# Performance work log

Hardware: AMD Instinct MI355X
Metric: run time of the kernel (lower is better)

## Reference

```python
import jax, jax.numpy as jnp
import numpy as np

INPUT_LEN = 256
LATENT = 128
B, T = 64, 1024
# layer (in_dim, units): encoder: (256,256),(256,128); decoder: (128,256),(256,256)
LAYERS = [(INPUT_LEN, 2 * LATENT), (2 * LATENT, LATENT), (LATENT, 2 * LATENT), (2 * LATENT, INPUT_LEN)]


def _lstm_relu(xs, W, U, b):
    """Keras LSTM with activation='relu', recurrent_activation='sigmoid'.
    xs: [B,T,F]; W: [F,4H]; U: [H,4H]; b: [4H]; gate order i,f,g,o. Returns [B,T,H]."""
    Bsz = xs.shape[0]
    H = U.shape[0]
    h0 = jnp.zeros((Bsz, H), xs.dtype)
    c0 = jnp.zeros((Bsz, H), xs.dtype)
    # precompute input projection for all timesteps: [T,B,4H]
    zx = jnp.einsum('btf,fg->tbg', xs, W) + b

    def step(carry, zx_t):
        h, c = carry
        z = zx_t + h @ U
        i, f, g, o = jnp.split(z, 4, axis=-1)
        i = jax.nn.sigmoid(i)
        f = jax.nn.sigmoid(f)
        o = jax.nn.sigmoid(o)
        g = jax.nn.relu(g)
        c = f * c + i * g
        h = o * jax.nn.relu(c)
        return (h, c), h

    _, hs = jax.lax.scan(step, (h0, c0), zx)  # hs: [T,B,H]
    return jnp.swapaxes(hs, 0, 1)


def setup_inputs() -> dict:
    key = jax.random.key(0)
    ks = jax.random.split(key, 1 + 3 * len(LAYERS))
    d = {"x": jax.random.normal(ks[0], (B, T, INPUT_LEN), dtype=jnp.float32)}
    for li, (fin, h) in enumerate(LAYERS):
        kW, kU, kb = ks[1 + 3 * li], ks[2 + 3 * li], ks[3 + 3 * li]
        d[f"W{li+1}"] = jax.random.normal(kW, (fin, 4 * h), dtype=jnp.float32) * 0.05
        d[f"U{li+1}"] = jax.random.normal(kU, (h, 4 * h), dtype=jnp.float32) * 0.05
        d[f"b{li+1}"] = jnp.zeros((4 * h,), dtype=jnp.float32)
    return d


def reference(x, W1, U1, b1, W2, U2, b2, W3, U3, b3, W4, U4, b4):
    h = _lstm_relu(x, W1, U1, b1)   # encoder layer 1: [B,T,256]
    h = _lstm_relu(h, W2, U2, b2)   # encoder layer 2: [B,T,128]
    h = _lstm_relu(h, W3, U3, b3)   # decoder layer 1: [B,T,256]
    h = _lstm_relu(h, W4, U4, b4)   # decoder layer 2: [B,T,256]
    return h
```

## Files before the change

### kernel.cpp

```cpp
#include <hip/hip_runtime.h>
#include <hip/hip_bf16.h>


typedef __bf16 bf16x8 __attribute__((ext_vector_type(8)));
typedef float f32x4 __attribute__((ext_vector_type(4)));

#define NWG 56
#define TSTEPS 1024
#define NSTEPS (TSTEPS + 3)

__device__ __forceinline__ f32x4 mfma16(bf16x8 a, bf16x8 b, f32x4 c) {
  return __builtin_amdgcn_mfma_f32_16x16x32_bf16(a, b, c, 0, 0, 0);
}

__device__ __forceinline__ float sigmoid_fast(float x) {
  return 1.0f / (1.0f + __expf(-x));
}

__device__ __forceinline__ void grid_barrier(unsigned* flags, int wg,
                                             unsigned target) {
  __syncthreads();
  if (threadIdx.x < 64) {
    __threadfence();
    if (threadIdx.x == 0)
      __hip_atomic_store(&flags[wg * 32], target, __ATOMIC_RELAXED,
                         __HIP_MEMORY_SCOPE_AGENT);
    const int idx = (threadIdx.x < NWG) ? (int)threadIdx.x : 0;
    while (true) {
      unsigned v = __hip_atomic_load(&flags[idx * 32], __ATOMIC_RELAXED,
                                     __HIP_MEMORY_SCOPE_AGENT);
      if (!__ballot(v < target)) break;
      __builtin_amdgcn_s_sleep(1);
    }
    __threadfence();
  }
  __syncthreads();
}

template <int F, int H, int LAYER>
__device__ void layer_loop(const float* __restrict__ xg,
                           const __bf16* __restrict__ xin,
                           const float* __restrict__ W,
                           const float* __restrict__ U,
                           const float* __restrict__ bias_g,
                           __bf16* __restrict__ hbuf,
                           float* __restrict__ out,
                           unsigned* flags, int wg, int slice, __bf16* smem) {
  constexpr int KW = F / 32;
  constexpr int KU = H / 32;
  constexpr int FOURH = 4 * H;
  const int tid = threadIdx.x;
  const int wave = tid >> 6;
  const int lane = tid & 63;
  const int l15 = lane & 15;
  const int q = lane >> 4;
  const int hcol = slice * 16 + l15;
  const int brow = wave * 16;

  float bz[4];
#pragma unroll
  for (int nt = 0; nt < 4; ++nt) bz[nt] = bias_g[nt * H + hcol];

  bf16x8 wf[4][KW];
  bf16x8 uf[4][KU];
  for (int idx = tid; idx < F * 64; idx += 256) {
    int k = idx >> 6, c = idx & 63;
    int col = (c >> 4) * H + slice * 16 + (c & 15);
    smem[c * F + k] = (__bf16)W[k * FOURH + col];
  }
  __syncthreads();
#pragma unroll
  for (int nt = 0; nt < 4; ++nt)
#pragma unroll
    for (int kk = 0; kk < KW; ++kk)
      wf[nt][kk] = *(const bf16x8*)&smem[(nt * 16 + l15) * F + kk * 32 + q * 8];
  __syncthreads();
  for (int idx = tid; idx < H * 64; idx += 256) {
    int k = idx >> 6, c = idx & 63;
    int col = (c >> 4) * H + slice * 16 + (c & 15);
    smem[c * H + k] = (__bf16)U[k * FOURH + col];
  }
  __syncthreads();
#pragma unroll
  for (int nt = 0; nt < 4; ++nt)
#pragma unroll
    for (int kk = 0; kk < KU; ++kk)
      uf[nt][kk] = *(const bf16x8*)&smem[(nt * 16 + l15) * H + kk * 32 + q * 8];

  float c_state[4] = {0.f, 0.f, 0.f, 0.f};

  for (int s = 0; s < NSTEPS; ++s) {
    const int t = s - (LAYER - 1);
    if (t >= 0 && t < TSTEPS) {
      f32x4 acc[4] = {};
      if (LAYER == 1) {
        const float* xrow = xg + ((size_t)(brow + l15) * 1024 + t) * 256 + q * 8;
#pragma unroll
        for (int kk = 0; kk < KW; ++kk) {
          const float4* p = (const float4*)(xrow + kk * 32);
          float4 a0 = p[0], a1 = p[1];
          bf16x8 a;
          a[0] = (__bf16)a0.x; a[1] = (__bf16)a0.y;
          a[2] = (__bf16)a0.z; a[3] = (__bf16)a0.w;
          a[4] = (__bf16)a1.x; a[5] = (__bf16)a1.y;
          a[6] = (__bf16)a1.z; a[7] = (__bf16)a1.w;
#pragma unroll
          for (int nt = 0; nt < 4; ++nt) acc[nt] = mfma16(a, wf[nt][kk], acc[nt]);
        }
      } else {
        const __bf16* xr = xin + ((size_t)(t & 1) * 64 + brow + l15) * F + q * 8;
#pragma unroll
        for (int kk = 0; kk < KW; ++kk) {
          bf16x8 a = *(const bf16x8*)(xr + kk * 32);
#pragma unroll
          for (int nt = 0; nt < 4; ++nt) acc[nt] = mfma16(a, wf[nt][kk], acc[nt]);
        }
      }
      if (t > 0) {
        const __bf16* hr = hbuf + ((size_t)((t - 1) & 1) * 64 + brow + l15) * H + q * 8;
#pragma unroll
        for (int kk = 0; kk < KU; ++kk) {
          bf16x8 a = *(const bf16x8*)(hr + kk * 32);
#pragma unroll
          for (int nt = 0; nt < 4; ++nt) acc[nt] = mfma16(a, uf[nt][kk], acc[nt]);
        }
      }
      __bf16* hw = hbuf + (size_t)(t & 1) * 64 * H;
#pragma unroll
      for (int r = 0; r < 4; ++r) {
        float zi = acc[0][r] + bz[0];
        float zf = acc[1][r] + bz[1];
        float zg = acc[2][r] + bz[2];
        float zo = acc[3][r] + bz[3];
        float ig = sigmoid_fast(zi);
        float fg = sigmoid_fast(zf);
        float gg = fmaxf(zg, 0.0f);
        float og = sigmoid_fast(zo);
        float cn = fg * c_state[r] + ig * gg;
        c_state[r] = cn;
        float hv = og * fmaxf(cn, 0.0f);
        int b = brow + q * 4 + r;
        hw[b * H + hcol] = (__bf16)hv;
        if (LAYER == 4) out[((size_t)b * 1024 + t) * 256 + hcol] = hv;
      }
    }
    grid_barrier(flags, wg, (unsigned)(s + 1));
  }
}

struct KParams {
  const float* x;
  const float* W1; const float* U1; const float* b1;
  const float* W2; const float* U2; const float* b2;
  const float* W3; const float* U3; const float* b3;
  const float* W4; const float* U4; const float* b4;
  float* out;
  unsigned* flags;
  void* h1; void* h2; void* h3; void* h4;
};

__global__ __launch_bounds__(256, 1) void lstm_kernel(KParams p) {
  __shared__ __align__(16) __bf16 smem[64 * 256];
  int wg = blockIdx.x;
  if (wg < 16)
    layer_loop<256, 256, 1>(p.x, nullptr, p.W1, p.U1, p.b1, (__bf16*)p.h1,
                            nullptr, p.flags, wg, wg, smem);
  else if (wg < 24)
    layer_loop<256, 128, 2>(nullptr, (const __bf16*)p.h1, p.W2, p.U2, p.b2,
                            (__bf16*)p.h2, nullptr, p.flags, wg, wg - 16, smem);
  else if (wg < 40)
    layer_loop<128, 256, 3>(nullptr, (const __bf16*)p.h2, p.W3, p.U3, p.b3,
                            (__bf16*)p.h3, nullptr, p.flags, wg, wg - 24, smem);
  else
    layer_loop<256, 256, 4>(nullptr, (const __bf16*)p.h3, p.W4, p.U4, p.b4,
                            (__bf16*)p.h4, p.out, p.flags, wg, wg - 40, smem);
}

extern "C" void kernel_launch(void* const* d_in, const int* in_sizes, int n_in,
                              void* d_out, int out_size, void* d_ws, size_t ws_size,
                              hipStream_t stream) {
  unsigned char* ws = (unsigned char*)d_ws;
  KParams p;
  p.x  = (const float*)d_in[0];
  p.W1 = (const float*)d_in[1];  p.U1 = (const float*)d_in[2];  p.b1 = (const float*)d_in[3];
  p.W2 = (const float*)d_in[4];  p.U2 = (const float*)d_in[5];  p.b2 = (const float*)d_in[6];
  p.W3 = (const float*)d_in[7];  p.U3 = (const float*)d_in[8];  p.b3 = (const float*)d_in[9];
  p.W4 = (const float*)d_in[10]; p.U4 = (const float*)d_in[11]; p.b4 = (const float*)d_in[12];
  p.out = (float*)d_out;
  p.flags = (unsigned*)ws;
  size_t off = 8192;
  p.h1 = (void*)(ws + off); off += (size_t)2 * 64 * 256 * 2;
  p.h2 = (void*)(ws + off); off += (size_t)2 * 64 * 128 * 2;
  p.h3 = (void*)(ws + off); off += (size_t)2 * 64 * 256 * 2;
  p.h4 = (void*)(ws + off);

  hipMemsetAsync(d_ws, 0, 8192, stream);

  lstm_kernel<<<dim3(NWG), dim3(256), 0, stream>>>(p);
}
```

Before: 9.254 ms.

## Replace fenced grid barrier with flag polling and agent-scope h exchange

Drops the heavyweight grid barrier and its two thread fences. Now every wave polls the per-workgroup step flags at the start of the step, and a single thread publishes the flag after the stores. Hidden-state exchange uses relaxed agent-scope atomic loads and stores so data is seen coherently across CUs without fences. h values are staged through LDS so they go out as coalesced 8-byte stores. The aim is to cut per-step synchronization latency in the 1027-step recurrence. The risk is memory ordering: with no release fence between the h stores and the flag store, a consumer could in principle read stale h.

```diff
diff --git a/kernel.cpp b/kernel.cpp
--- a/kernel.cpp
+++ b/kernel.cpp
@@ -4,6 +4,7 @@
 
 typedef __bf16 bf16x8 __attribute__((ext_vector_type(8)));
 typedef float f32x4 __attribute__((ext_vector_type(4)));
+typedef unsigned long long u64;
 
 #define NWG 56
 #define TSTEPS 1024
@@ -17,24 +18,28 @@
   return 1.0f / (1.0f + __expf(-x));
 }
 
-__device__ __forceinline__ void grid_barrier(unsigned* flags, int wg,
-                                             unsigned target) {
-  __syncthreads();
-  if (threadIdx.x < 64) {
-    __threadfence();
-    if (threadIdx.x == 0)
-      __hip_atomic_store(&flags[wg * 32], target, __ATOMIC_RELAXED,
-                         __HIP_MEMORY_SCOPE_AGENT);
-    const int idx = (threadIdx.x < NWG) ? (int)threadIdx.x : 0;
-    while (true) {
-      unsigned v = __hip_atomic_load(&flags[idx * 32], __ATOMIC_RELAXED,
-                                     __HIP_MEMORY_SCOPE_AGENT);
-      if (!__ballot(v < target)) break;
-      __builtin_amdgcn_s_sleep(1);
-    }
-    __threadfence();
-  }
-  __syncthreads();
+__device__ __forceinline__ bf16x8 load_frag_llc(const __bf16* p) {
+  union { bf16x8 v; u64 d[2]; } u;
+  u.d[0] = __hip_atomic_load((const u64*)p, __ATOMIC_RELAXED,
+                             __HIP_MEMORY_SCOPE_AGENT);
+  u.d[1] = __hip_atomic_load((const u64*)(p + 4), __ATOMIC_RELAXED,
+                             __HIP_MEMORY_SCOPE_AGENT);
+  return u.v;
+}
+
+__device__ __forceinline__ void store8_llc(__bf16* p, u64 v) {
+  __hip_atomic_store((u64*)p, v, __ATOMIC_RELAXED, __HIP_MEMORY_SCOPE_AGENT);
+}
+
+__device__ __forceinline__ void poll_flags(unsigned* flags, unsigned s) {
+  const int lane = threadIdx.x & 63;
+  const int idx = (lane < NWG) ? lane : 0;
+  while (true) {
+    unsigned v = __hip_atomic_load(&flags[idx * 32], __ATOMIC_RELAXED,
+                                   __HIP_MEMORY_SCOPE_AGENT);
+    if (!__ballot(v < s)) break;
+    __builtin_amdgcn_s_sleep(1);
+  }
 }
 
 template <int F, int H, int LAYER>
@@ -86,12 +91,18 @@
 #pragma unroll
     for (int kk = 0; kk < KU; ++kk)
       uf[nt][kk] = *(const bf16x8*)&smem[(nt * 16 + l15) * H + kk * 32 + q * 8];
+  __syncthreads();
+
+  __bf16* hlds = smem;
 
   float c_state[4] = {0.f, 0.f, 0.f, 0.f};
 
   for (int s = 0; s < NSTEPS; ++s) {
     const int t = s - (LAYER - 1);
-    if (t >= 0 && t < TSTEPS) {
+    const bool active = (t >= 0) & (t < TSTEPS);
+    poll_flags(flags, (unsigned)s);
+    float hv[4];
+    if (active) {
       f32x4 acc[4] = {};
       if (LAYER == 1) {
         const float* xrow = xg + ((size_t)(brow + l15) * 1024 + t) * 256 + q * 8;
@@ -111,7 +122,7 @@
         const __bf16* xr = xin + ((size_t)(t & 1) * 64 + brow + l15) * F + q * 8;
 #pragma unroll
         for (int kk = 0; kk < KW; ++kk) {
-          bf16x8 a = *(const bf16x8*)(xr + kk * 32);
+          bf16x8 a = load_frag_llc(xr + kk * 32);
 #pragma unroll
           for (int nt = 0; nt < 4; ++nt) acc[nt] = mfma16(a, wf[nt][kk], acc[nt]);
         }
@@ -120,12 +131,11 @@
         const __bf16* hr = hbuf + ((size_t)((t - 1) & 1) * 64 + brow + l15) * H + q * 8;
 #pragma unroll
         for (int kk = 0; kk < KU; ++kk) {
-          bf16x8 a = *(const bf16x8*)(hr + kk * 32);
+          bf16x8 a = load_frag_llc(hr + kk * 32);
 #pragma unroll
           for (int nt = 0; nt < 4; ++nt) acc[nt] = mfma16(a, uf[nt][kk], acc[nt]);
         }
       }
-      __bf16* hw = hbuf + (size_t)(t & 1) * 64 * H;
 #pragma unroll
       for (int r = 0; r < 4; ++r) {
         float zi = acc[0][r] + bz[0];
@@ -138,13 +148,27 @@
         float og = sigmoid_fast(zo);
         float cn = fg * c_state[r] + ig * gg;
         c_state[r] = cn;
-        float hv = og * fmaxf(cn, 0.0f);
-        int b = brow + q * 4 + r;
-        hw[b * H + hcol] = (__bf16)hv;
-        if (LAYER == 4) out[((size_t)b * 1024 + t) * 256 + hcol] = hv;
+        hv[r] = og * fmaxf(cn, 0.0f);
+        hlds[(brow + q * 4 + r) * 16 + l15] = (__bf16)hv[r];
       }
     }
-    grid_barrier(flags, wg, (unsigned)(s + 1));
+    __syncthreads();
+    if (active) {
+      int row = tid >> 2, cg = tid & 3;
+      u64 v = *(const u64*)&hlds[row * 16 + cg * 4];
+      store8_llc(hbuf + ((size_t)(t & 1) * 64 + row) * H + slice * 16 + cg * 4, v);
+      if (LAYER == 4) {
+#pragma unroll
+        for (int r = 0; r < 4; ++r) {
+          int b = brow + q * 4 + r;
+          out[((size_t)b * 1024 + t) * 256 + hcol] = hv[r];
+        }
+      }
+    }
+    __syncthreads();
+    if (tid == 0)
+      __hip_atomic_store(&flags[wg * 32], (unsigned)(s + 1), __ATOMIC_RELAXED,
+                         __HIP_MEMORY_SCOPE_AGENT);
   }
 }
 
```

After: 8.022 ms. -13.3%, faster.
